# Optimization experiments

Measured on AMD Instinct MI355X. Metric: run time of the kernel, lower is better.

The kernel has to match this reference:

```python
import jax, jax.numpy as jnp
import numpy as np

D_MODEL = 1024
N_HEADS = 16
D_K = D_MODEL // N_HEADS
B, S = 2, 2048


def setup_inputs() -> dict:
    key = jax.random.key(0)
    ks = jax.random.split(key, 5)
    sc = 1.0 / np.sqrt(D_MODEL)
    return {
        "x": jax.random.normal(ks[0], (B, S, D_MODEL), dtype=jnp.float32),
        "W_qkv": jax.random.normal(ks[1], (D_MODEL, 3 * D_MODEL), dtype=jnp.float32) * sc,
        "b_qkv": jnp.zeros((3 * D_MODEL,), dtype=jnp.float32),
        "W_out": jax.random.normal(ks[2], (D_MODEL, D_MODEL), dtype=jnp.float32) * sc,
        "b_out": jnp.zeros((D_MODEL,), dtype=jnp.float32),
    }


def reference(x, W_qkv, b_qkv, W_out, b_out):
    Bb, Ss, _ = x.shape
    qkv = x @ W_qkv + b_qkv                     # [B,S,3*D]
    qkv = qkv.reshape(Bb, Ss, 3, N_HEADS, D_K)
    qkv = jnp.transpose(qkv, (2, 0, 3, 1, 4))   # [3,B,H,S,Dk]
    q, k, v = qkv[0], qkv[1], qkv[2]
    scale = jnp.asarray(np.sqrt(D_K), dtype=x.dtype)
    attn = jnp.einsum('bhsd,bhtd->bhst', q, k) / scale  # [B,H,S,S]
    attn = jax.nn.softmax(attn, axis=-1)
    out = jnp.einsum('bhst,bhtd->bhsd', attn, v)        # [B,H,S,Dk]
    out = jnp.transpose(out, (0, 2, 1, 3)).reshape(Bb, Ss, D_MODEL)
    return out @ W_out + b_out
```

## Files before the change

### kernel.cpp

```cpp
#include <hip/hip_runtime.h>

typedef __bf16 bf16x8 __attribute__((ext_vector_type(8)));
typedef __bf16 bf16x4 __attribute__((ext_vector_type(4)));
typedef __bf16 bf16x2 __attribute__((ext_vector_type(2)));
typedef float f32x4 __attribute__((ext_vector_type(4)));
typedef unsigned short u16;
typedef unsigned short u16x4 __attribute__((ext_vector_type(4)));
typedef unsigned short u16x8 __attribute__((ext_vector_type(8)));
typedef unsigned int u32;
typedef unsigned int u32x2 __attribute__((ext_vector_type(2)));
typedef unsigned int u32x4 __attribute__((ext_vector_type(4)));

__device__ __forceinline__ u16 f2bu(float f) {
  __bf16 h = (__bf16)f;
  return __builtin_bit_cast(u16, h);
}

__device__ __forceinline__ void gld16(const u16* g, const __bf16* lds) {
  __builtin_amdgcn_global_load_lds(
      (const __attribute__((address_space(1))) u32*)(uintptr_t)g,
      (__attribute__((address_space(3))) u32*)(u32)(uintptr_t)lds, 16, 0, 0);
}

__device__ __forceinline__ void tr_tile(const float* __restrict__ in, u16* __restrict__ out,
                                        int R, int C, int bx, int by, int tid) {
  __shared__ u16 t[64][65];
  int tx = tid & 63, ty = tid >> 6;
  int r0 = by * 64, c0 = bx * 64;
  for (int i = 0; i < 16; ++i)
    t[ty + i * 4][tx] = f2bu(in[(size_t)(r0 + ty + i * 4) * C + c0 + tx]);
  __syncthreads();
  for (int i = 0; i < 16; ++i)
    out[(size_t)(c0 + ty + i * 4) * R + r0 + tx] = t[tx][ty + i * 4];
}

__global__ __launch_bounds__(256) void prep(const float* __restrict__ Wqkv,
                                            u16* __restrict__ Wqkv_t,
                                            const float* __restrict__ Wout,
                                            u16* __restrict__ Wout_t,
                                            const float* __restrict__ x,
                                            u16* __restrict__ xb) {
  int id = blockIdx.x, tid = threadIdx.x;
  if (id < 768) {
    tr_tile(Wqkv, Wqkv_t, 1024, 3072, id % 48, id / 48, tid);
  } else if (id < 1024) {
    int id2 = id - 768;
    tr_tile(Wout, Wout_t, 1024, 1024, id2 % 16, id2 / 16, tid);
  } else {
    size_t i = ((size_t)(id - 1024) * 256 + tid) * 8;
    f32x4 a0 = *(const f32x4*)(x + i);
    f32x4 a1 = *(const f32x4*)(x + i + 4);
    bf16x8 v;
    for (int j = 0; j < 4; ++j) { v[j] = (__bf16)a0[j]; v[j + 4] = (__bf16)a1[j]; }
    *(bf16x8*)(xb + i) = v;
  }
}

template <int MODE, int TM, int TN, int MT, int NT, int XM, int XN>
__global__ __launch_bounds__(256) void gemm_bt(const u16* __restrict__ A,
                                               const u16* __restrict__ Bt,
                                               const float* __restrict__ bias,
                                               void* __restrict__ O0v,
                                               u16* __restrict__ O1,
                                               u16* __restrict__ O2,
                                               int M, int N, int K) {
  constexpr int NI = TM / 32;
  constexpr int NJ = TN / 32;
  constexpr int AE = TM * 32;
  constexpr int BE = TN * 32;
  __shared__ __bf16 smem[2 * (AE + BE)];

  int tid = threadIdx.x;
  int w = tid >> 6, lane = tid & 63, quad = lane >> 4, l16 = lane & 15;
  int wr = w >> 1, wc = w & 1;

  int id = blockIdx.x;
  int xcd = id & 7, s0i = id >> 3;
  int mg = xcd % (MT / XM), ng = xcd / (MT / XM);
  int sm = s0i % XM, sn = s0i / XM;
  int m0 = (mg * XM + sm) * TM, n0 = (ng * XN + sn) * TN;

  int srow = w * 16 + (lane >> 2);
  int sch = (lane & 3) ^ ((lane >> 3) & 3);
  const u16* Ag = A + (size_t)(m0 + srow) * K + sch * 8;
  const u16* Bg = Bt + (size_t)(n0 + srow) * K + sch * 8;

  int swl = (quad ^ ((l16 >> 1) & 3)) << 3;

  f32x4 acc[NI][NJ] = {};

#define GLD_STEP(c, kk)                                                          \
  {                                                                              \
    for (int p = 0; p < TM / 64; ++p)                                            \
      gld16(Ag + (size_t)p * 64 * K + (kk), smem + (c) * (AE + BE) + w * 512 + p * 2048); \
    for (int p = 0; p < TN / 64; ++p)                                            \
      gld16(Bg + (size_t)p * 64 * K + (kk), smem + (c) * (AE + BE) + AE + w * 512 + p * 2048); \
  }

  GLD_STEP(0, 0);
  int NS = K / 32;
  for (int s = 0; s < NS; ++s) {
    int cur = s & 1;
    __syncthreads();
    if (s + 1 < NS) GLD_STEP(1 - cur, (s + 1) * 32);
    const __bf16* Asub = smem + cur * (AE + BE);
    const __bf16* Bsub = Asub + AE;
    bf16x8 af[NI], bfr[NJ];
    for (int i = 0; i < NI; ++i)
      af[i] = *(const bf16x8*)(Asub + (wr * (TM / 2) + i * 16 + l16) * 32 + swl);
    for (int j = 0; j < NJ; ++j)
      bfr[j] = *(const bf16x8*)(Bsub + (wc * (TN / 2) + j * 16 + l16) * 32 + swl);
    for (int i = 0; i < NI; ++i)
      for (int j = 0; j < NJ; ++j)
        acc[i][j] = __builtin_amdgcn_mfma_f32_16x16x32_bf16(af[i], bfr[j], acc[i][j], 0, 0, 0);
  }
#undef GLD_STEP

  if (MODE == 0) {
    float* O0 = (float*)O0v;
    for (int j = 0; j < NJ; ++j) {
      int n = n0 + wc * (TN / 2) + j * 16 + l16;
      float bv = bias[n];
      for (int i = 0; i < NI; ++i) {
        int mb = m0 + wr * (TM / 2) + i * 16 + quad * 4;
        for (int r = 0; r < 4; ++r)
          O0[(size_t)(mb + r) * N + n] = acc[i][j][r] + bv;
      }
    }
  } else {
    constexpr float QSC = 0.125f * 1.44269504f;
    int bw = n0 >> 10;
    if (bw < 2) {
      u16* Od = bw ? O1 : (u16*)O0v;
      float sc = bw ? 1.f : QSC;
      __syncthreads();
      u16* Ls = (u16*)smem;
      for (int j = 0; j < NJ; ++j) {
        int col = wc * (TN / 2) + j * 16 + l16;
        float bv = bias[n0 + col];
        for (int i = 0; i < NI; ++i) {
          int rowb = wr * (TM / 2) + i * 16 + quad * 4;
          for (int r = 0; r < 4; ++r) {
            int row = rowb + r;
            Ls[(size_t)row * TN + (col ^ ((row & 7) << 4))] = f2bu((acc[i][j][r] + bv) * sc);
          }
        }
      }
      __syncthreads();
      for (int k = 0; k < TM * TN / 8 / 256; ++k) {
        int ch = tid + k * 256;
        int row = ch >> 4, col0 = (ch & 15) * 8;
        u16x8 v8 = *(const u16x8*)(Ls + (size_t)row * TN + (col0 ^ ((row & 7) << 4)));
        int m = m0 + row;
        int b = m >> 11, s = m & 2047;
        int n = n0 + col0;
        int h = (n & 1023) >> 6, d0 = n & 63;
        *(u16x8*)(Od + (((size_t)(b * 16 + h)) * 2048 + s) * 64 + d0) = v8;
      }
    } else {
      for (int j = 0; j < NJ; ++j) {
        int n = n0 + wc * (TN / 2) + j * 16 + l16;
        int h = (n & 1023) >> 6, d = n & 63;
        float bv = bias[n];
        for (int pr = 0; pr < NI / 2; ++pr) {
          const f32x4& e = acc[2 * pr][j];
          const f32x4& f = acc[2 * pr + 1][j];
          bf16x2 e01 = {(__bf16)(e[0] + bv), (__bf16)(e[1] + bv)};
          bf16x2 e23 = {(__bf16)(e[2] + bv), (__bf16)(e[3] + bv)};
          bf16x2 f01 = {(__bf16)(f[0] + bv), (__bf16)(f[1] + bv)};
          bf16x2 f23 = {(__bf16)(f[2] + bv), (__bf16)(f[3] + bv)};
          u32 E[2] = {__builtin_bit_cast(u32, e01), __builtin_bit_cast(u32, e23)};
          u32 F[2] = {__builtin_bit_cast(u32, f01), __builtin_bit_cast(u32, f23)};
          u32 G[2], H[2];
          for (int w2 = 0; w2 < 2; ++w2) {
            u32x2 s1 = __builtin_amdgcn_permlane32_swap(E[w2], F[w2], false, false);
            u32x2 s2 = __builtin_amdgcn_permlane16_swap(s1[0], s1[1], false, false);
            G[w2] = s2[0];
            H[w2] = s2[1];
          }
          u32x4 pk = {G[0], G[1], H[0], H[1]};
          int m = m0 + wr * (TM / 2) + pr * 32 + quad * 8;
          int b = m >> 11, s = m & 2047;
          *(u32x4*)(O2 + (((size_t)(b * 16 + h)) * 64 + d) * 2048 + s) = pk;
        }
      }
    }
  }
}

__global__ __launch_bounds__(512, 4) void flash_attn(const u16* __restrict__ Q,
                                                     const u16* __restrict__ K,
                                                     const u16* __restrict__ Vt,
                                                     u16* __restrict__ AO) {
  constexpr int S = 2048;
  constexpr int HALF = S / 2;
  constexpr int NIT = HALF / 64;
  __shared__ __bf16 lds[2][2][2][64 * 64];

  int bh = blockIdx.x, qbase = blockIdx.y * 128;
  int tid = threadIdx.x;
  int grp = tid >> 8, gtid = tid & 255;
  int w = gtid >> 6, lane = tid & 63, quad = lane >> 4, l16 = lane & 15;

  const u16* Qh = Q + (size_t)bh * S * 64;
  const u16* Kh = K + (size_t)bh * S * 64 + (size_t)grp * HALF * 64;
  const u16* Vh = Vt + (size_t)bh * 64 * S + grp * HALF;

  int qrowA = qbase + w * 32 + l16;
  int qrowB = qrowA + 16;
  bf16x8 qf0a = *(const bf16x8*)(Qh + (size_t)qrowA * 64 + quad * 8);
  bf16x8 qf1a = *(const bf16x8*)(Qh + (size_t)qrowA * 64 + 32 + quad * 8);
  bf16x8 qf0b = *(const bf16x8*)(Qh + (size_t)qrowB * 64 + quad * 8);
  bf16x8 qf1b = *(const bf16x8*)(Qh + (size_t)qrowB * 64 + 32 + quad * 8);

  bf16x8 vone;
#pragma unroll
  for (int j = 0; j < 8; ++j) vone[j] = (__bf16)1.0f;

  __bf16* Ks0 = &lds[grp][0][0][0];
  __bf16* Vs0 = &lds[grp][1][0][0];

  int lrow = lane >> 3, lgr = lane & 7;
  int sgr = (lgr ^ lrow) << 3;
  const u16* Ksrc = Kh + ((size_t)(w * 16) + lrow) * 64 + sgr;
  const u16* Vsrc = Vh + ((size_t)(w * 16) + lrow) * S + sgr;
  const __bf16* Kdst = Ks0 + w * 16 * 64;
  const __bf16* Vdst = Vs0 + w * 16 * 64;

#define STAGE(c, tb)                                                    \
  {                                                                     \
    gld16(Ksrc + (size_t)(tb) * 64, Kdst + (c) * 4096);                 \
    gld16(Ksrc + (size_t)((tb) + 8) * 64, Kdst + (c) * 4096 + 512);     \
    gld16(Vsrc + (tb), Vdst + (c) * 4096);                              \
    gld16(Vsrc + (size_t)8 * S + (tb), Vdst + (c) * 4096 + 512);        \
  }

  STAGE(0, 0);
  __syncthreads();

  f32x4 oA[4] = {};
  f32x4 oB[4] = {};
  f32x4 lfA = {};
  f32x4 lfB = {};
  int xr = l16 & 7;

  for (int it = 0; it < NIT; ++it) {
    int c = it & 1;
    if (it + 1 < NIT) STAGE(1 - c, (it + 1) * 64);

    u32 pwA[4][2], pwB[4][2];
#pragma unroll
    for (int nt = 0; nt < 4; ++nt) {
      const __bf16* kb = Ks0 + c * 4096 + (nt * 16 + l16) * 64;
      bf16x8 kf0 = *(const bf16x8*)(kb + ((quad ^ xr) << 3));
      bf16x8 kf1 = *(const bf16x8*)(kb + (((quad + 4) ^ xr) << 3));
      f32x4 ca = {0.f, 0.f, 0.f, 0.f};
      f32x4 cb = {0.f, 0.f, 0.f, 0.f};
      __builtin_amdgcn_s_setprio(1);
      ca = __builtin_amdgcn_mfma_f32_16x16x32_bf16(kf0, qf0a, ca, 0, 0, 0);
      cb = __builtin_amdgcn_mfma_f32_16x16x32_bf16(kf0, qf0b, cb, 0, 0, 0);
      ca = __builtin_amdgcn_mfma_f32_16x16x32_bf16(kf1, qf1a, ca, 0, 0, 0);
      cb = __builtin_amdgcn_mfma_f32_16x16x32_bf16(kf1, qf1b, cb, 0, 0, 0);
      __builtin_amdgcn_s_setprio(0);
      bf16x2 a01 = {(__bf16)__builtin_amdgcn_exp2f(ca[0]), (__bf16)__builtin_amdgcn_exp2f(ca[1])};
      bf16x2 a23 = {(__bf16)__builtin_amdgcn_exp2f(ca[2]), (__bf16)__builtin_amdgcn_exp2f(ca[3])};
      bf16x2 b01 = {(__bf16)__builtin_amdgcn_exp2f(cb[0]), (__bf16)__builtin_amdgcn_exp2f(cb[1])};
      bf16x2 b23 = {(__bf16)__builtin_amdgcn_exp2f(cb[2]), (__bf16)__builtin_amdgcn_exp2f(cb[3])};
      pwA[nt][0] = __builtin_bit_cast(u32, a01);
      pwA[nt][1] = __builtin_bit_cast(u32, a23);
      pwB[nt][0] = __builtin_bit_cast(u32, b01);
      pwB[nt][1] = __builtin_bit_cast(u32, b23);
    }

    bf16x8 pfA[2], pfB[2];
#pragma unroll
    for (int h = 0; h < 2; ++h) {
      u32 GA[2], HA[2], GB[2], HB[2];
#pragma unroll
      for (int w2 = 0; w2 < 2; ++w2) {
        u32x2 s1a = __builtin_amdgcn_permlane32_swap(pwA[2 * h][w2], pwA[2 * h + 1][w2], false, false);
        u32x2 s2a = __builtin_amdgcn_permlane16_swap(s1a[0], s1a[1], false, false);
        GA[w2] = s2a[0];
        HA[w2] = s2a[1];
        u32x2 s1b = __builtin_amdgcn_permlane32_swap(pwB[2 * h][w2], pwB[2 * h + 1][w2], false, false);
        u32x2 s2b = __builtin_amdgcn_permlane16_swap(s1b[0], s1b[1], false, false);
        GB[w2] = s2b[0];
        HB[w2] = s2b[1];
      }
      u32x4 pa = {GA[0], GA[1], HA[0], HA[1]};
      u32x4 pb = {GB[0], GB[1], HB[0], HB[1]};
      pfA[h] = __builtin_bit_cast(bf16x8, pa);
      pfB[h] = __builtin_bit_cast(bf16x8, pb);
    }

    __builtin_amdgcn_s_setprio(1);
    lfA = __builtin_amdgcn_mfma_f32_16x16x32_bf16(pfA[0], vone, lfA, 0, 0, 0);
    lfA = __builtin_amdgcn_mfma_f32_16x16x32_bf16(pfA[1], vone, lfA, 0, 0, 0);
    lfB = __builtin_amdgcn_mfma_f32_16x16x32_bf16(pfB[0], vone, lfB, 0, 0, 0);
    lfB = __builtin_amdgcn_mfma_f32_16x16x32_bf16(pfB[1], vone, lfB, 0, 0, 0);
    __builtin_amdgcn_s_setprio(0);

#pragma unroll
    for (int dt = 0; dt < 4; ++dt) {
      const __bf16* vb = Vs0 + c * 4096 + (dt * 16 + l16) * 64;
      bf16x8 v0 = *(const bf16x8*)(vb + ((quad ^ xr) << 3));
      bf16x8 v1 = *(const bf16x8*)(vb + (((quad + 4) ^ xr) << 3));
      __builtin_amdgcn_s_setprio(1);
      oA[dt] = __builtin_amdgcn_mfma_f32_16x16x32_bf16(pfA[0], v0, oA[dt], 0, 0, 0);
      oB[dt] = __builtin_amdgcn_mfma_f32_16x16x32_bf16(pfB[0], v0, oB[dt], 0, 0, 0);
      oA[dt] = __builtin_amdgcn_mfma_f32_16x16x32_bf16(pfA[1], v1, oA[dt], 0, 0, 0);
      oB[dt] = __builtin_amdgcn_mfma_f32_16x16x32_bf16(pfB[1], v1, oB[dt], 0, 0, 0);
      __builtin_amdgcn_s_setprio(0);
    }
    __syncthreads();
  }
#undef STAGE

  float* mf = (float*)&lds[0][0][0][0];
  if (grp) {
    float* p = mf + (size_t)gtid * 41;
#pragma unroll
    for (int dt = 0; dt < 4; ++dt)
#pragma unroll
      for (int r = 0; r < 4; ++r) {
        p[dt * 4 + r] = oA[dt][r];
        p[16 + dt * 4 + r] = oB[dt][r];
      }
#pragma unroll
    for (int r = 0; r < 4; ++r) {
      p[32 + r] = lfA[r];
      p[36 + r] = lfB[r];
    }
  }
  __syncthreads();
  if (!grp) {
    const float* p = mf + (size_t)gtid * 41;
    float linvA[4], linvB[4];
#pragma unroll
    for (int r = 0; r < 4; ++r) {
      linvA[r] = 1.f / (lfA[r] + p[32 + r]);
      linvB[r] = 1.f / (lfB[r] + p[36 + r]);
    }
    int b = bh >> 4, h = bh & 15;
    for (int dt = 0; dt < 4; ++dt)
      for (int r = 0; r < 4; ++r) {
        int sA = qbase + w * 32 + quad * 4 + r;
        int sB = sA + 16;
        int d = dt * 16 + l16;
        AO[(((size_t)b * 2048 + sA) * 16 + h) * 64 + d] = f2bu((oA[dt][r] + p[dt * 4 + r]) * linvA[r]);
        AO[(((size_t)b * 2048 + sB) * 16 + h) * 64 + d] = f2bu((oB[dt][r] + p[16 + dt * 4 + r]) * linvB[r]);
      }
  }
}

extern "C" void kernel_launch(void* const* d_in, const int* in_sizes, int n_in,
                              void* d_out, int out_size, void* d_ws, size_t ws_size,
                              hipStream_t stream) {
  const float* x    = (const float*)d_in[0];
  const float* Wqkv = (const float*)d_in[1];
  const float* bqkv = (const float*)d_in[2];
  const float* Wout = (const float*)d_in[3];
  const float* bout = (const float*)d_in[4];
  float* out = (float*)d_out;

  u16* ws = (u16*)d_ws;
  size_t off = 0;
  u16* Wqkv_t = ws + off; off += (size_t)3072 * 1024;
  u16* Wout_t = ws + off; off += (size_t)1024 * 1024;
  u16* xb     = ws + off; off += (size_t)4096 * 1024;
  u16* Qb     = ws + off; off += (size_t)32 * 2048 * 64;
  u16* Kb     = ws + off; off += (size_t)32 * 2048 * 64;
  u16* Vtb    = ws + off; off += (size_t)32 * 2048 * 64;
  u16* AO     = xb;

  prep<<<dim3(3072), 256, 0, stream>>>(Wqkv, Wqkv_t, Wout, Wout_t, x, xb);
  gemm_bt<1, 128, 128, 32, 24, 8, 12><<<dim3(768), 256, 0, stream>>>(
      xb, Wqkv_t, bqkv, (void*)Qb, Kb, Vtb, 4096, 3072, 1024);
  flash_attn<<<dim3(32, 16), 512, 0, stream>>>(Qb, Kb, Vtb, AO);
  gemm_bt<0, 128, 64, 32, 16, 8, 8><<<dim3(512), 256, 0, stream>>>(
      AO, Wout_t, bout, (void*)out, nullptr, nullptr, 4096, 1024, 1024);
}
```

Measured before the change: 176.2 us.

## Split flash attention KV range across four wave groups with 32-wide tiles

The attention kernel now uses 1024-thread blocks. Its KV sequence is split into four quarters instead of two halves, and each group processes KV tiles of 32 keys instead of 64, with new swizzled staging into LDS. Partial outputs and row sums are combined in a multi-step LDS reduction (pairs first, then the final two groups). The goal is more waves per CU for latency hiding and a shorter per-group serial KV loop. In exchange it adds extra barriers and reduction traffic, shrinks per-iteration MFMA work, and the aggressive launch bounds may cap registers and cause spills.

```diff
diff --git a/kernel.cpp b/kernel.cpp
--- a/kernel.cpp
+++ b/kernel.cpp
@@ -188,14 +188,15 @@
   }
 }
 
-__global__ __launch_bounds__(512, 4) void flash_attn(const u16* __restrict__ Q,
-                                                     const u16* __restrict__ K,
-                                                     const u16* __restrict__ Vt,
-                                                     u16* __restrict__ AO) {
+__global__ __launch_bounds__(1024, 8) void flash_attn(const u16* __restrict__ Q,
+                                                      const u16* __restrict__ K,
+                                                      const u16* __restrict__ Vt,
+                                                      u16* __restrict__ AO) {
   constexpr int S = 2048;
-  constexpr int HALF = S / 2;
-  constexpr int NIT = HALF / 64;
-  __shared__ __bf16 lds[2][2][2][64 * 64];
+  constexpr int QTR = S / 4;
+  constexpr int KVB = 32;
+  constexpr int NIT = QTR / KVB;
+  __shared__ __bf16 lds[4][2][2][KVB * 64];
 
   int bh = blockIdx.x, qbase = blockIdx.y * 128;
   int tid = threadIdx.x;
@@ -203,8 +204,8 @@
   int w = gtid >> 6, lane = tid & 63, quad = lane >> 4, l16 = lane & 15;
 
   const u16* Qh = Q + (size_t)bh * S * 64;
-  const u16* Kh = K + (size_t)bh * S * 64 + (size_t)grp * HALF * 64;
-  const u16* Vh = Vt + (size_t)bh * 64 * S + grp * HALF;
+  const u16* Kh = K + (size_t)bh * S * 64 + (size_t)grp * QTR * 64;
+  const u16* Vh = Vt + (size_t)bh * 64 * S + grp * QTR;
 
   int qrowA = qbase + w * 32 + l16;
   int qrowB = qrowA + 16;
@@ -217,22 +218,17 @@
 #pragma unroll
   for (int j = 0; j < 8; ++j) vone[j] = (__bf16)1.0f;
 
-  __bf16* Ks0 = &lds[grp][0][0][0];
-  __bf16* Vs0 = &lds[grp][1][0][0];
-
-  int lrow = lane >> 3, lgr = lane & 7;
-  int sgr = (lgr ^ lrow) << 3;
-  const u16* Ksrc = Kh + ((size_t)(w * 16) + lrow) * 64 + sgr;
-  const u16* Vsrc = Vh + ((size_t)(w * 16) + lrow) * S + sgr;
-  const __bf16* Kdst = Ks0 + w * 16 * 64;
-  const __bf16* Vdst = Vs0 + w * 16 * 64;
-
-#define STAGE(c, tb)                                                    \
-  {                                                                     \
-    gld16(Ksrc + (size_t)(tb) * 64, Kdst + (c) * 4096);                 \
-    gld16(Ksrc + (size_t)((tb) + 8) * 64, Kdst + (c) * 4096 + 512);     \
-    gld16(Vsrc + (tb), Vdst + (c) * 4096);                              \
-    gld16(Vsrc + (size_t)8 * S + (tb), Vdst + (c) * 4096 + 512);        \
+  int lrK = lane >> 3;
+  const u16* Ksrc = Kh + ((size_t)(w * 8 + lrK)) * 64 + (((lane & 7) ^ lrK) << 3);
+  int lrV = lane >> 2;
+  const u16* Vsrc = Vh + ((size_t)(w * 16 + lrV)) * S + (((lane & 3) ^ ((lane >> 3) & 3)) << 3);
+  const __bf16* Kdst = &lds[grp][0][0][0] + w * 512;
+  const __bf16* Vdst = &lds[grp][1][0][0] + w * 512;
+
+#define STAGE(c, tb)                                     \
+  {                                                      \
+    gld16(Ksrc + (size_t)(tb) * 64, Kdst + (c) * 2048);  \
+    gld16(Vsrc + (tb), Vdst + (c) * 2048);               \
   }
 
   STAGE(0, 0);
@@ -243,15 +239,18 @@
   f32x4 lfA = {};
   f32x4 lfB = {};
   int xr = l16 & 7;
+  int xv = (l16 >> 1) & 3;
+  const __bf16* Kb0 = &lds[grp][0][0][0];
+  const __bf16* Vb0 = &lds[grp][1][0][0];
 
   for (int it = 0; it < NIT; ++it) {
     int c = it & 1;
-    if (it + 1 < NIT) STAGE(1 - c, (it + 1) * 64);
-
-    u32 pwA[4][2], pwB[4][2];
-#pragma unroll
-    for (int nt = 0; nt < 4; ++nt) {
-      const __bf16* kb = Ks0 + c * 4096 + (nt * 16 + l16) * 64;
+    if (it + 1 < NIT) STAGE(1 - c, (it + 1) * KVB);
+
+    u32 pwA[2][2], pwB[2][2];
+#pragma unroll
+    for (int nt = 0; nt < 2; ++nt) {
+      const __bf16* kb = Kb0 + c * 2048 + (nt * 16 + l16) * 64;
       bf16x8 kf0 = *(const bf16x8*)(kb + ((quad ^ xr) << 3));
       bf16x8 kf1 = *(const bf16x8*)(kb + (((quad + 4) ^ xr) << 3));
       f32x4 ca = {0.f, 0.f, 0.f, 0.f};
@@ -272,44 +271,38 @@
       pwB[nt][1] = __builtin_bit_cast(u32, b23);
     }
 
-    bf16x8 pfA[2], pfB[2];
-#pragma unroll
-    for (int h = 0; h < 2; ++h) {
+    bf16x8 pfA, pfB;
+    {
       u32 GA[2], HA[2], GB[2], HB[2];
 #pragma unroll
       for (int w2 = 0; w2 < 2; ++w2) {
-        u32x2 s1a = __builtin_amdgcn_permlane32_swap(pwA[2 * h][w2], pwA[2 * h + 1][w2], false, false);
+        u32x2 s1a = __builtin_amdgcn_permlane32_swap(pwA[0][w2], pwA[1][w2], false, false);
         u32x2 s2a = __builtin_amdgcn_permlane16_swap(s1a[0], s1a[1], false, false);
         GA[w2] = s2a[0];
         HA[w2] = s2a[1];
-        u32x2 s1b = __builtin_amdgcn_permlane32_swap(pwB[2 * h][w2], pwB[2 * h + 1][w2], false, false);
+        u32x2 s1b = __builtin_amdgcn_permlane32_swap(pwB[0][w2], pwB[1][w2], false, false);
         u32x2 s2b = __builtin_amdgcn_permlane16_swap(s1b[0], s1b[1], false, false);
         GB[w2] = s2b[0];
         HB[w2] = s2b[1];
       }
       u32x4 pa = {GA[0], GA[1], HA[0], HA[1]};
       u32x4 pb = {GB[0], GB[1], HB[0], HB[1]};
-      pfA[h] = __builtin_bit_cast(bf16x8, pa);
-      pfB[h] = __builtin_bit_cast(bf16x8, pb);
+      pfA = __builtin_bit_cast(bf16x8, pa);
+      pfB = __builtin_bit_cast(bf16x8, pb);
     }
 
     __builtin_amdgcn_s_setprio(1);
-    lfA = __builtin_amdgcn_mfma_f32_16x16x32_bf16(pfA[0], vone, lfA, 0, 0, 0);
-    lfA = __builtin_amdgcn_mfma_f32_16x16x32_bf16(pfA[1], vone, lfA, 0, 0, 0);
-    lfB = __builtin_amdgcn_mfma_f32_16x16x32_bf16(pfB[0], vone, lfB, 0, 0, 0);
-    lfB = __builtin_amdgcn_mfma_f32_16x16x32_bf16(pfB[1], vone, lfB, 0, 0, 0);
+    lfA = __builtin_amdgcn_mfma_f32_16x16x32_bf16(pfA, vone, lfA, 0, 0, 0);
+    lfB = __builtin_amdgcn_mfma_f32_16x16x32_bf16(pfB, vone, lfB, 0, 0, 0);
     __builtin_amdgcn_s_setprio(0);
 
 #pragma unroll
     for (int dt = 0; dt < 4; ++dt) {
-      const __bf16* vb = Vs0 + c * 4096 + (dt * 16 + l16) * 64;
-      bf16x8 v0 = *(const bf16x8*)(vb + ((quad ^ xr) << 3));
-      bf16x8 v1 = *(const bf16x8*)(vb + (((quad + 4) ^ xr) << 3));
+      const __bf16* vb = Vb0 + c * 2048 + (dt * 16 + l16) * 32;
+      bf16x8 v0 = *(const bf16x8*)(vb + ((quad ^ xv) << 3));
       __builtin_amdgcn_s_setprio(1);
-      oA[dt] = __builtin_amdgcn_mfma_f32_16x16x32_bf16(pfA[0], v0, oA[dt], 0, 0, 0);
-      oB[dt] = __builtin_amdgcn_mfma_f32_16x16x32_bf16(pfB[0], v0, oB[dt], 0, 0, 0);
-      oA[dt] = __builtin_amdgcn_mfma_f32_16x16x32_bf16(pfA[1], v1, oA[dt], 0, 0, 0);
-      oB[dt] = __builtin_amdgcn_mfma_f32_16x16x32_bf16(pfB[1], v1, oB[dt], 0, 0, 0);
+      oA[dt] = __builtin_amdgcn_mfma_f32_16x16x32_bf16(pfA, v0, oA[dt], 0, 0, 0);
+      oB[dt] = __builtin_amdgcn_mfma_f32_16x16x32_bf16(pfB, v0, oB[dt], 0, 0, 0);
       __builtin_amdgcn_s_setprio(0);
     }
     __syncthreads();
@@ -317,7 +310,47 @@
 #undef STAGE
 
   float* mf = (float*)&lds[0][0][0][0];
-  if (grp) {
+  if (grp & 1) {
+    float* p = mf + (size_t)((grp >> 1) * 256 + gtid) * 21;
+#pragma unroll
+    for (int dt = 0; dt < 4; ++dt)
+#pragma unroll
+      for (int r = 0; r < 4; ++r) p[dt * 4 + r] = oA[dt][r];
+#pragma unroll
+    for (int r = 0; r < 4; ++r) p[16 + r] = lfA[r];
+  }
+  __syncthreads();
+  if (!(grp & 1)) {
+    const float* p = mf + (size_t)((grp >> 1) * 256 + gtid) * 21;
+#pragma unroll
+    for (int dt = 0; dt < 4; ++dt)
+#pragma unroll
+      for (int r = 0; r < 4; ++r) oA[dt][r] += p[dt * 4 + r];
+#pragma unroll
+    for (int r = 0; r < 4; ++r) lfA[r] += p[16 + r];
+  }
+  __syncthreads();
+  if (grp & 1) {
+    float* p = mf + (size_t)((grp >> 1) * 256 + gtid) * 21;
+#pragma unroll
+    for (int dt = 0; dt < 4; ++dt)
+#pragma unroll
+      for (int r = 0; r < 4; ++r) p[dt * 4 + r] = oB[dt][r];
+#pragma unroll
+    for (int r = 0; r < 4; ++r) p[16 + r] = lfB[r];
+  }
+  __syncthreads();
+  if (!(grp & 1)) {
+    const float* p = mf + (size_t)((grp >> 1) * 256 + gtid) * 21;
+#pragma unroll
+    for (int dt = 0; dt < 4; ++dt)
+#pragma unroll
+      for (int r = 0; r < 4; ++r) oB[dt][r] += p[dt * 4 + r];
+#pragma unroll
+    for (int r = 0; r < 4; ++r) lfB[r] += p[16 + r];
+  }
+  __syncthreads();
+  if (grp == 2) {
     float* p = mf + (size_t)gtid * 41;
 #pragma unroll
     for (int dt = 0; dt < 4; ++dt)
@@ -333,7 +366,7 @@
     }
   }
   __syncthreads();
-  if (!grp) {
+  if (grp == 0) {
     const float* p = mf + (size_t)gtid * 41;
     float linvA[4], linvB[4];
 #pragma unroll
@@ -376,7 +409,7 @@
   prep<<<dim3(3072), 256, 0, stream>>>(Wqkv, Wqkv_t, Wout, Wout_t, x, xb);
   gemm_bt<1, 128, 128, 32, 24, 8, 12><<<dim3(768), 256, 0, stream>>>(
       xb, Wqkv_t, bqkv, (void*)Qb, Kb, Vtb, 4096, 3072, 1024);
-  flash_attn<<<dim3(32, 16), 512, 0, stream>>>(Qb, Kb, Vtb, AO);
+  flash_attn<<<dim3(32, 16), 1024, 0, stream>>>(Qb, Kb, Vtb, AO);
   gemm_bt<0, 128, 64, 32, 16, 8, 8><<<dim3(512), 256, 0, stream>>>(
       AO, Wout_t, bout, (void*)out, nullptr, nullptr, 4096, 1024, 1024);
 }
```

Measured after the change: 437.4 us. +148.3%, slower.
